# Kernel optimization log

Hardware: AMD Instinct MI355X
Metric: run time of the kernel (lower is better)

Reference implementation:

```python
import jax, jax.numpy as jnp
import numpy as np

HIDDEN = 1024
HEADS = 16
HEAD_DIM = HIDDEN // HEADS


def setup_inputs() -> dict:
    key = jax.random.key(0)
    ks = jax.random.split(key, 9)
    s = 1.0 / np.sqrt(HIDDEN)
    inp = {
        "x": jax.random.normal(ks[0], (4, 2048, HIDDEN), dtype=jnp.float32),
        "wq": jax.random.uniform(ks[1], (HIDDEN, HIDDEN), jnp.float32, -s, s),
        "bq": jax.random.uniform(ks[2], (HIDDEN,), jnp.float32, -s, s),
        "wk": jax.random.uniform(ks[3], (HIDDEN, HIDDEN), jnp.float32, -s, s),
        "bk": jax.random.uniform(ks[4], (HIDDEN,), jnp.float32, -s, s),
        "wv": jax.random.uniform(ks[5], (HIDDEN, HIDDEN), jnp.float32, -s, s),
        "bv": jax.random.uniform(ks[6], (HIDDEN,), jnp.float32, -s, s),
        "wo": jax.random.uniform(ks[7], (HIDDEN, HIDDEN), jnp.float32, -s, s),
        "bo": jax.random.uniform(ks[8], (HIDDEN,), jnp.float32, -s, s),
    }
    return inp


def reference(x, wq, bq, wk, bk, wv, bv, wo, bo):
    B, S, D = x.shape
    H, Hd = HEADS, HEAD_DIM
    # torch Linear: y = x @ W.T + b
    def split_heads(t):  # [B,S,D] -> [B,H,S,Hd]
        return t.reshape(B, S, H, Hd).transpose(0, 2, 1, 3)
    q = split_heads(x @ wq.T + bq)
    k = split_heads(x @ wk.T + bk)
    v = split_heads(x @ wv.T + bv)
    scores = jnp.einsum('bhqd,bhkd->bhqk', q, k) / jnp.sqrt(jnp.float32(Hd))
    attn = jax.nn.softmax(scores, axis=-1)  # dropout is identity in eval
    ctx = jnp.einsum('bhqk,bhkd->bhqd', attn, v)
    ctx = ctx.transpose(0, 2, 1, 3).reshape(B, S, D)
    pooled = ctx.mean(axis=1)  # [B, D]
    out = pooled @ wo.T + bo
    return out, attn.mean(axis=1)
```

## Files before the change

### kernel.cpp

```cpp
#include <hip/hip_runtime.h>

#define B_ 4
#define S_ 2048
#define D_ 1024
#define H_ 16
#define HD_ 64
#define M_ 8192

typedef __attribute__((ext_vector_type(8))) short          bf16x8;
typedef __attribute__((ext_vector_type(8))) unsigned short u16x8;
typedef __attribute__((ext_vector_type(4))) float          f32x4;

#define MFMA16(a, b, c) __builtin_amdgcn_mfma_f32_16x16x32_bf16((a), (b), (c), 0, 0, 0)

#define SCL 0.18033688011112042f

__device__ __forceinline__ unsigned short f2b(float f) {
    unsigned int u = __float_as_uint(f);
    return (unsigned short)((u + 0x7fffu + ((u >> 16) & 1u)) >> 16);
}

__device__ __forceinline__ unsigned int cvtpk_bf16(float lo, float hi) {
    unsigned int r;
    asm("v_cvt_pk_bf16_f32 %0, %1, %2" : "=v"(r) : "v"(lo), "v"(hi));
    return r;
}

__global__ __launch_bounds__(256) void cast_k(const float* __restrict__ src,
                                              unsigned short* __restrict__ dst, int n) {
    int i = (blockIdx.x * 256 + threadIdx.x) * 4;
    if (i >= n) return;
    float4 v = *(const float4*)(src + i);
    ushort4 o;
    o.x = f2b(v.x); o.y = f2b(v.y); o.z = f2b(v.z); o.w = f2b(v.w);
    *(ushort4*)(dst + i) = o;
}

__global__ __launch_bounds__(256) void cast3_k(
    const float* __restrict__ s0, const float* __restrict__ s1, const float* __restrict__ s2,
    unsigned short* __restrict__ d0, unsigned short* __restrict__ d1,
    unsigned short* __restrict__ d2, int n) {
    const float* src = (blockIdx.y == 0) ? s0 : (blockIdx.y == 1) ? s1 : s2;
    unsigned short* dst = (blockIdx.y == 0) ? d0 : (blockIdx.y == 1) ? d1 : d2;
    int i = (blockIdx.x * 256 + threadIdx.x) * 4;
    if (i >= n) return;
    float4 v = *(const float4*)(src + i);
    ushort4 o;
    o.x = f2b(v.x); o.y = f2b(v.y); o.z = f2b(v.z); o.w = f2b(v.w);
    *(ushort4*)(dst + i) = o;
}

__global__ __launch_bounds__(256) void qkv_gemm_k(
    const unsigned short* __restrict__ xb,
    const unsigned short* __restrict__ wb0, const unsigned short* __restrict__ wb1,
    const unsigned short* __restrict__ wb2,
    const float* __restrict__ bq, const float* __restrict__ bk, const float* __restrict__ bv,
    unsigned short* __restrict__ Qo, unsigned short* __restrict__ Ko,
    unsigned short* __restrict__ Vo)
{
    __shared__ unsigned short xs[128][72];
    __shared__ unsigned short wsm[128][72];

    const unsigned short* W; const float* bias; unsigned short* out;
    if (blockIdx.z == 0)      { W = wb0; bias = bq; out = Qo; }
    else if (blockIdx.z == 1) { W = wb1; bias = bk; out = Ko; }
    else                      { W = wb2; bias = bv; out = Vo; }
    const float oscale = (blockIdx.z == 0) ? SCL : 1.0f;

    const int m0 = blockIdx.x * 128, n0 = blockIdx.y * 128;
    const int tid = threadIdx.x, lane = tid & 63, wid = tid >> 6;
    const int wm = (wid >> 1) * 64, wn = (wid & 1) * 64;
    const int srow = tid >> 3;
    const int skc  = (tid & 7) * 8;

    f32x4 acc[4][4] = {};

    for (int k0 = 0; k0 < D_; k0 += 64) {
        u16x8 xa[4], wa[4];
        #pragma unroll
        for (int r = 0; r < 4; ++r) {
            int row = srow + 32 * r;
            xa[r] = *(const u16x8*)&xb[(size_t)(m0 + row) * D_ + k0 + skc];
            wa[r] = *(const u16x8*)&W [(size_t)(n0 + row) * D_ + k0 + skc];
        }
        __syncthreads();
        #pragma unroll
        for (int r = 0; r < 4; ++r) {
            int row = srow + 32 * r;
            *(u16x8*)&xs[row][skc]  = xa[r];
            *(u16x8*)&wsm[row][skc] = wa[r];
        }
        __syncthreads();
        #pragma unroll
        for (int kd = 0; kd < 2; ++kd) {
            const int kc = 32 * kd + 8 * (lane >> 4);
            bf16x8 af[4], bfr[4];
            #pragma unroll
            for (int mf = 0; mf < 4; ++mf)
                af[mf] = *(const bf16x8*)&xs[wm + 16 * mf + (lane & 15)][kc];
            #pragma unroll
            for (int nf = 0; nf < 4; ++nf)
                bfr[nf] = *(const bf16x8*)&wsm[wn + 16 * nf + (lane & 15)][kc];
            #pragma unroll
            for (int mf = 0; mf < 4; ++mf)
                #pragma unroll
                for (int nf = 0; nf < 4; ++nf)
                    acc[mf][nf] = MFMA16(af[mf], bfr[nf], acc[mf][nf]);
        }
    }

    const int col_l = lane & 15, rgrp = lane >> 4;
    #pragma unroll
    for (int nf = 0; nf < 4; ++nf) {
        const int n = n0 + wn + 16 * nf + col_l;
        const float bval = bias[n];
        const int h = n >> 6, d = n & 63;
        #pragma unroll
        for (int mf = 0; mf < 4; ++mf)
            #pragma unroll
            for (int r = 0; r < 4; ++r) {
                int m = m0 + wm + 16 * mf + 4 * rgrp + r;
                int bI = m >> 11, s = m & 2047;
                out[(((size_t)bI * H_ + h) * S_ + s) * HD_ + d]
                    = f2b((acc[mf][nf][r] + bval) * oscale);
            }
    }
}

__global__ __launch_bounds__(256) void attn_ctx_k(
    const unsigned short* __restrict__ Q, const unsigned short* __restrict__ K,
    const unsigned short* __restrict__ V,
    float* __restrict__ L, float* __restrict__ PPOOL)
{
    __shared__ unsigned short ks[64][72];
    __shared__ unsigned short vt[64][72];
    __shared__ unsigned short ps[128][72];
    __shared__ float pp[4][64];
    __shared__ float lsm[4][32];

    const int q0 = blockIdx.x * 128, h = blockIdx.y, b = blockIdx.z;
    const size_t hoff = ((size_t)(b * H_ + h)) * S_ * HD_;
    const unsigned short* Qh = Q + hoff;
    const unsigned short* Kh = K + hoff;
    const unsigned short* Vh = V + hoff;

    const int tid = threadIdx.x, lane = tid & 63, wid = tid >> 6;
    const int srow = tid >> 3;
    const int skc  = (tid & 7) * 8;
    const int col_l = lane & 15, rgrp = lane >> 4;

    bf16x8 qf[2][2];
    #pragma unroll
    for (int i = 0; i < 2; ++i)
        #pragma unroll
        for (int kd = 0; kd < 2; ++kd)
            qf[i][kd] = *(const bf16x8*)&Qh[(size_t)(q0 + 32 * wid + 16 * i + col_l) * HD_
                                            + 32 * kd + 8 * rgrp];

    f32x4 cacc[2][4] = {};
    float lp[2] = {};

    for (int kb = 0; kb < S_; kb += 64) {
        u16x8 ka[2], va[2];
        #pragma unroll
        for (int r = 0; r < 2; ++r) {
            int row = srow + 32 * r;
            ka[r] = *(const u16x8*)&Kh[(size_t)(kb + row) * HD_ + skc];
            va[r] = *(const u16x8*)&Vh[(size_t)(kb + row) * HD_ + skc];
        }
        __syncthreads();
        #pragma unroll
        for (int r = 0; r < 2; ++r) {
            int row = srow + 32 * r;
            *(u16x8*)&ks[row][skc] = ka[r];
            #pragma unroll
            for (int j = 0; j < 8; ++j)
                vt[skc + j][row] = va[r][j];
        }
        __syncthreads();

        #pragma unroll
        for (int n = 0; n < 4; ++n) {
            f32x4 s0 = {}, s1 = {};
            #pragma unroll
            for (int kd = 0; kd < 2; ++kd) {
                const int kc = 32 * kd + 8 * rgrp;
                bf16x8 kf = *(const bf16x8*)&ks[16 * n + col_l][kc];
                s0 = MFMA16(kf, qf[0][kd], s0);
                s1 = MFMA16(kf, qf[1][kd], s1);
            }
            float e0 = exp2f(s0[0]), e1 = exp2f(s0[1]), e2 = exp2f(s0[2]), e3 = exp2f(s0[3]);
            lp[0] += (e0 + e1) + (e2 + e3);
            uint2 w0 = { cvtpk_bf16(e0, e1), cvtpk_bf16(e2, e3) };
            *(uint2*)&ps[32 * wid + col_l][16 * n + 4 * rgrp] = w0;
            float f0 = exp2f(s1[0]), f1 = exp2f(s1[1]), f2 = exp2f(s1[2]), f3 = exp2f(s1[3]);
            lp[1] += (f0 + f1) + (f2 + f3);
            uint2 w1 = { cvtpk_bf16(f0, f1), cvtpk_bf16(f2, f3) };
            *(uint2*)&ps[32 * wid + 16 + col_l][16 * n + 4 * rgrp] = w1;
        }

        #pragma unroll
        for (int kk = 0; kk < 2; ++kk) {
            const int kc = 32 * kk + 8 * rgrp;
            bf16x8 pa[2], vf[4];
            #pragma unroll
            for (int i = 0; i < 2; ++i)
                pa[i] = *(const bf16x8*)&ps[32 * wid + 16 * i + col_l][kc];
            #pragma unroll
            for (int n = 0; n < 4; ++n)
                vf[n] = *(const bf16x8*)&vt[16 * n + col_l][kc];
            #pragma unroll
            for (int i = 0; i < 2; ++i)
                #pragma unroll
                for (int n = 0; n < 4; ++n)
                    cacc[i][n] = MFMA16(pa[i], vf[n], cacc[i][n]);
        }
    }

    #pragma unroll
    for (int i = 0; i < 2; ++i) {
        float v = lp[i];
        v += __shfl_xor(v, 16); v += __shfl_xor(v, 32);
        lp[i] = v;
    }
    if (lane < 16) {
        #pragma unroll
        for (int i = 0; i < 2; ++i) {
            L[((size_t)(b * H_ + h)) * S_ + q0 + 32 * wid + 16 * i + lane] = lp[i];
            lsm[wid][16 * i + lane] = lp[i];
        }
    }

    float pool4[4] = {};
    #pragma unroll
    for (int i = 0; i < 2; ++i)
        #pragma unroll
        for (int r = 0; r < 4; ++r) {
            float inv = 1.0f / lsm[wid][16 * i + 4 * rgrp + r];
            #pragma unroll
            for (int n = 0; n < 4; ++n)
                pool4[n] = fmaf(cacc[i][n][r], inv, pool4[n]);
        }
    #pragma unroll
    for (int n = 0; n < 4; ++n) {
        float v = pool4[n];
        v += __shfl_xor(v, 16); v += __shfl_xor(v, 32);
        pool4[n] = v;
    }
    if (lane < 16) {
        #pragma unroll
        for (int n = 0; n < 4; ++n) pp[wid][16 * n + lane] = pool4[n];
    }
    __syncthreads();
    if (tid < 64) {
        float s = pp[0][tid] + pp[1][tid] + pp[2][tid] + pp[3][tid];
        PPOOL[((size_t)(b * H_ + h) * (S_ / 128) + blockIdx.x) * 64 + tid] = s;
    }
}

__global__ __launch_bounds__(256) void attn_mean_k(
    const unsigned short* __restrict__ Q, const unsigned short* __restrict__ K,
    const float* __restrict__ L, float* __restrict__ attn_out)
{
    __shared__ unsigned short qs[128][72];
    __shared__ unsigned short ksm[64][72];
    __shared__ float lsm[128];

    const int k0 = blockIdx.x * 64, q0 = blockIdx.y * 128, b = blockIdx.z;
    const int tid = threadIdx.x, lane = tid & 63, wid = tid >> 6;
    const int col_l = lane & 15, rgrp = lane >> 4;
    const int qrow = tid >> 1, qcol = (tid & 1) * 32;
    const int krow = tid >> 2, kcol = (tid & 3) * 16;

    f32x4 macc[4][2] = {};

    for (int h = 0; h < H_; ++h) {
        const size_t hoff = ((size_t)(b * H_ + h)) * S_ * HD_;
        const unsigned short* Qh = Q + hoff;
        const unsigned short* Kh = K + hoff;

        u16x8 qa[4], ka[2];
        #pragma unroll
        for (int j = 0; j < 4; ++j)
            qa[j] = *(const u16x8*)&Qh[(size_t)(q0 + qrow) * HD_ + qcol + 8 * j];
        #pragma unroll
        for (int j = 0; j < 2; ++j)
            ka[j] = *(const u16x8*)&Kh[(size_t)(k0 + krow) * HD_ + kcol + 8 * j];
        float lval = 0.f;
        if (tid < 128) lval = L[((size_t)(b * H_ + h)) * S_ + q0 + tid];

        __syncthreads();
        #pragma unroll
        for (int j = 0; j < 4; ++j) *(u16x8*)&qs[qrow][qcol + 8 * j] = qa[j];
        #pragma unroll
        for (int j = 0; j < 2; ++j) *(u16x8*)&ksm[krow][kcol + 8 * j] = ka[j];
        if (tid < 128) lsm[tid] = lval;
        __syncthreads();

        bf16x8 qf[2][2];
        #pragma unroll
        for (int i = 0; i < 2; ++i)
            #pragma unroll
            for (int kd = 0; kd < 2; ++kd)
                qf[i][kd] = *(const bf16x8*)&qs[32 * wid + 16 * i + col_l][32 * kd + 8 * rgrp];

        float li0 = 0.0625f / lsm[32 * wid + col_l];
        float li1 = 0.0625f / lsm[32 * wid + 16 + col_l];

        #pragma unroll
        for (int n = 0; n < 4; ++n) {
            f32x4 s0 = {}, s1 = {};
            #pragma unroll
            for (int kd = 0; kd < 2; ++kd) {
                bf16x8 kf = *(const bf16x8*)&ksm[16 * n + col_l][32 * kd + 8 * rgrp];
                s0 = MFMA16(kf, qf[0][kd], s0);
                s1 = MFMA16(kf, qf[1][kd], s1);
            }
            #pragma unroll
            for (int r = 0; r < 4; ++r) {
                macc[n][0][r] = fmaf(exp2f(s0[r]), li0, macc[n][0][r]);
                macc[n][1][r] = fmaf(exp2f(s1[r]), li1, macc[n][1][r]);
            }
        }
    }

    #pragma unroll
    for (int n = 0; n < 4; ++n)
        #pragma unroll
        for (int i = 0; i < 2; ++i) {
            int q = q0 + 32 * wid + 16 * i + col_l;
            *(f32x4*)&attn_out[((size_t)b * S_ + q) * S_ + k0 + 16 * n + 4 * rgrp]
                = macc[n][i];
        }
}

__global__ __launch_bounds__(256) void out_k(
    const float* __restrict__ PPOOL, const float* __restrict__ wo,
    const float* __restrict__ bo, float* __restrict__ out)
{
    __shared__ float psm[D_];
    const int b = blockIdx.x >> 2;
    for (int d = threadIdx.x; d < D_; d += 256) {
        const float* pp = PPOOL + ((size_t)(b * H_ + (d >> 6)) * (S_ / 128)) * 64 + (d & 63);
        float s = 0.f;
        #pragma unroll
        for (int qb = 0; qb < S_ / 128; ++qb) s += pp[qb * 64];
        psm[d] = s * (1.0f / S_);
    }
    __syncthreads();
    const int j = (blockIdx.x & 3) * 256 + threadIdx.x;
    float sum = bo[j];
    const float* wr = wo + (size_t)j * D_;
    for (int d = 0; d < D_; d += 4) {
        float4 w4 = *(const float4*)&wr[d];
        sum += psm[d] * w4.x + psm[d+1] * w4.y + psm[d+2] * w4.z + psm[d+3] * w4.w;
    }
    out[b * D_ + j] = sum;
}

extern "C" void kernel_launch(void* const* d_in, const int* in_sizes, int n_in,
                              void* d_out, int out_size, void* d_ws, size_t ws_size,
                              hipStream_t stream)
{
    const float* x  = (const float*)d_in[0];
    const float* wq = (const float*)d_in[1];
    const float* bq = (const float*)d_in[2];
    const float* wk = (const float*)d_in[3];
    const float* bk = (const float*)d_in[4];
    const float* wv = (const float*)d_in[5];
    const float* bv = (const float*)d_in[6];
    const float* wo = (const float*)d_in[7];
    const float* bo = (const float*)d_in[8];
    float* out = (float*)d_out;

    char* ws = (char*)d_ws;
    const size_t XN  = (size_t)M_ * D_;
    const size_t WN  = (size_t)D_ * D_;
    const size_t QN  = (size_t)B_ * H_ * S_ * HD_;

    unsigned short* xb  = (unsigned short*)ws;                 ws += XN * 2;
    unsigned short* wqb = (unsigned short*)ws;                 ws += WN * 2;
    unsigned short* wkb = (unsigned short*)ws;                 ws += WN * 2;
    unsigned short* wvb = (unsigned short*)ws;                 ws += WN * 2;
    unsigned short* Qb  = (unsigned short*)ws;                 ws += QN * 2;
    unsigned short* Kb  = (unsigned short*)ws;                 ws += QN * 2;
    unsigned short* Vb  = (unsigned short*)ws;                 ws += QN * 2;
    float* Lb    = (float*)ws;                                 ws += (size_t)B_ * H_ * S_ * 4;
    float* PPOOL = (float*)ws;

    cast_k<<<dim3(XN / 1024), 256, 0, stream>>>(x, xb, (int)XN);
    cast3_k<<<dim3(WN / 1024, 3), 256, 0, stream>>>(wq, wk, wv, wqb, wkb, wvb, (int)WN);

    qkv_gemm_k<<<dim3(M_ / 128, D_ / 128, 3), 256, 0, stream>>>(
        xb, wqb, wkb, wvb, bq, bk, bv, Qb, Kb, Vb);
    attn_ctx_k<<<dim3(S_ / 128, H_, B_), 256, 0, stream>>>(Qb, Kb, Vb, Lb, PPOOL);
    attn_mean_k<<<dim3(S_ / 64, S_ / 128, B_), 256, 0, stream>>>(Qb, Kb, Lb, out + B_ * D_);
    out_k<<<16, 256, 0, stream>>>(PPOOL, wo, bo, out);
}
```

Before: 438.2 us.

## Write V pre-transposed from QKV GEMM and swizzle attention block order

The QKV GEMM now writes V in a [B,H,HD,S] transposed layout with 4-wide vector stores, so the attention kernel can load V tiles straight into shared memory with vector stores instead of a scalar per-element transpose. The attention grid is also flattened to 1D and remapped so that groups of 8 heads run alongside each other, which is meant to improve L2 reuse of K/V across query blocks. The cost is a differently strided epilogue in the GEMM for the V slice.

```diff
diff --git a/kernel.cpp b/kernel.cpp
--- a/kernel.cpp
+++ b/kernel.cpp
@@ -56,16 +56,15 @@
     const unsigned short* __restrict__ wb2,
     const float* __restrict__ bq, const float* __restrict__ bk, const float* __restrict__ bv,
     unsigned short* __restrict__ Qo, unsigned short* __restrict__ Ko,
-    unsigned short* __restrict__ Vo)
+    unsigned short* __restrict__ VT)
 {
     __shared__ unsigned short xs[128][72];
     __shared__ unsigned short wsm[128][72];
 
-    const unsigned short* W; const float* bias; unsigned short* out;
-    if (blockIdx.z == 0)      { W = wb0; bias = bq; out = Qo; }
-    else if (blockIdx.z == 1) { W = wb1; bias = bk; out = Ko; }
-    else                      { W = wb2; bias = bv; out = Vo; }
-    const float oscale = (blockIdx.z == 0) ? SCL : 1.0f;
+    const unsigned short* W; const float* bias;
+    if (blockIdx.z == 0)      { W = wb0; bias = bq; }
+    else if (blockIdx.z == 1) { W = wb1; bias = bk; }
+    else                      { W = wb2; bias = bv; }
 
     const int m0 = blockIdx.x * 128, n0 = blockIdx.y * 128;
     const int tid = threadIdx.x, lane = tid & 63, wid = tid >> 6;
@@ -110,26 +109,48 @@
     }
 
     const int col_l = lane & 15, rgrp = lane >> 4;
-    #pragma unroll
-    for (int nf = 0; nf < 4; ++nf) {
-        const int n = n0 + wn + 16 * nf + col_l;
-        const float bval = bias[n];
-        const int h = n >> 6, d = n & 63;
-        #pragma unroll
-        for (int mf = 0; mf < 4; ++mf)
-            #pragma unroll
-            for (int r = 0; r < 4; ++r) {
-                int m = m0 + wm + 16 * mf + 4 * rgrp + r;
+    if (blockIdx.z != 2) {
+        unsigned short* out = (blockIdx.z == 0) ? Qo : Ko;
+        const float oscale = (blockIdx.z == 0) ? SCL : 1.0f;
+        #pragma unroll
+        for (int nf = 0; nf < 4; ++nf) {
+            const int n = n0 + wn + 16 * nf + col_l;
+            const float bval = bias[n];
+            const int h = n >> 6, d = n & 63;
+            #pragma unroll
+            for (int mf = 0; mf < 4; ++mf)
+                #pragma unroll
+                for (int r = 0; r < 4; ++r) {
+                    int m = m0 + wm + 16 * mf + 4 * rgrp + r;
+                    int bI = m >> 11, s = m & 2047;
+                    out[(((size_t)bI * H_ + h) * S_ + s) * HD_ + d]
+                        = f2b((acc[mf][nf][r] + bval) * oscale);
+                }
+        }
+    } else {
+        #pragma unroll
+        for (int nf = 0; nf < 4; ++nf) {
+            const int n = n0 + wn + 16 * nf + col_l;
+            const float bval = bias[n];
+            const int h = n >> 6, d = n & 63;
+            #pragma unroll
+            for (int mf = 0; mf < 4; ++mf) {
+                int m = m0 + wm + 16 * mf + 4 * rgrp;
                 int bI = m >> 11, s = m & 2047;
-                out[(((size_t)bI * H_ + h) * S_ + s) * HD_ + d]
-                    = f2b((acc[mf][nf][r] + bval) * oscale);
+                ushort4 o;
+                o.x = f2b(acc[mf][nf][0] + bval);
+                o.y = f2b(acc[mf][nf][1] + bval);
+                o.z = f2b(acc[mf][nf][2] + bval);
+                o.w = f2b(acc[mf][nf][3] + bval);
+                *(ushort4*)&VT[(((size_t)bI * H_ + h) * HD_ + d) * S_ + s] = o;
             }
+        }
     }
 }
 
 __global__ __launch_bounds__(256) void attn_ctx_k(
     const unsigned short* __restrict__ Q, const unsigned short* __restrict__ K,
-    const unsigned short* __restrict__ V,
+    const unsigned short* __restrict__ VT,
     float* __restrict__ L, float* __restrict__ PPOOL)
 {
     __shared__ unsigned short ks[64][72];
@@ -138,11 +159,16 @@
     __shared__ float pp[4][64];
     __shared__ float lsm[4][32];
 
-    const int q0 = blockIdx.x * 128, h = blockIdx.y, b = blockIdx.z;
+    const int lin = blockIdx.x;
+    const int g   = (lin & 7) | ((lin >> 7) << 3);
+    const int qb  = (lin >> 3) & 15;
+    const int b   = g >> 4, h = g & 15;
+    const int q0  = qb * 128;
+
     const size_t hoff = ((size_t)(b * H_ + h)) * S_ * HD_;
-    const unsigned short* Qh = Q + hoff;
-    const unsigned short* Kh = K + hoff;
-    const unsigned short* Vh = V + hoff;
+    const unsigned short* Qh  = Q  + hoff;
+    const unsigned short* Kh  = K  + hoff;
+    const unsigned short* VTh = VT + hoff;
 
     const int tid = threadIdx.x, lane = tid & 63, wid = tid >> 6;
     const int srow = tid >> 3;
@@ -165,17 +191,15 @@
         #pragma unroll
         for (int r = 0; r < 2; ++r) {
             int row = srow + 32 * r;
-            ka[r] = *(const u16x8*)&Kh[(size_t)(kb + row) * HD_ + skc];
-            va[r] = *(const u16x8*)&Vh[(size_t)(kb + row) * HD_ + skc];
+            ka[r] = *(const u16x8*)&Kh [(size_t)(kb + row) * HD_ + skc];
+            va[r] = *(const u16x8*)&VTh[(size_t)row * S_ + kb + skc];
         }
         __syncthreads();
         #pragma unroll
         for (int r = 0; r < 2; ++r) {
             int row = srow + 32 * r;
             *(u16x8*)&ks[row][skc] = ka[r];
-            #pragma unroll
-            for (int j = 0; j < 8; ++j)
-                vt[skc + j][row] = va[r][j];
+            *(u16x8*)&vt[row][skc] = va[r];
         }
         __syncthreads();
 
@@ -254,7 +278,7 @@
     __syncthreads();
     if (tid < 64) {
         float s = pp[0][tid] + pp[1][tid] + pp[2][tid] + pp[3][tid];
-        PPOOL[((size_t)(b * H_ + h) * (S_ / 128) + blockIdx.x) * 64 + tid] = s;
+        PPOOL[((size_t)(b * H_ + h) * (S_ / 128) + qb) * 64 + tid] = s;
     }
 }
 
@@ -384,7 +408,7 @@
     unsigned short* wvb = (unsigned short*)ws;                 ws += WN * 2;
     unsigned short* Qb  = (unsigned short*)ws;                 ws += QN * 2;
     unsigned short* Kb  = (unsigned short*)ws;                 ws += QN * 2;
-    unsigned short* Vb  = (unsigned short*)ws;                 ws += QN * 2;
+    unsigned short* VTb = (unsigned short*)ws;                 ws += QN * 2;
     float* Lb    = (float*)ws;                                 ws += (size_t)B_ * H_ * S_ * 4;
     float* PPOOL = (float*)ws;
 
@@ -392,8 +416,8 @@
     cast3_k<<<dim3(WN / 1024, 3), 256, 0, stream>>>(wq, wk, wv, wqb, wkb, wvb, (int)WN);
 
     qkv_gemm_k<<<dim3(M_ / 128, D_ / 128, 3), 256, 0, stream>>>(
-        xb, wqb, wkb, wvb, bq, bk, bv, Qb, Kb, Vb);
-    attn_ctx_k<<<dim3(S_ / 128, H_, B_), 256, 0, stream>>>(Qb, Kb, Vb, Lb, PPOOL);
+        xb, wqb, wkb, wvb, bq, bk, bv, Qb, Kb, VTb);
+    attn_ctx_k<<<dim3(1024), 256, 0, stream>>>(Qb, Kb, VTb, Lb, PPOOL);
     attn_mean_k<<<dim3(S_ / 64, S_ / 128, B_), 256, 0, stream>>>(Qb, Kb, Lb, out + B_ * D_);
     out_k<<<16, 256, 0, stream>>>(PPOOL, wo, bo, out);
 }
```

Result: faster. 404.1 us (-7.8%).
